# Performance work log

Hardware: AMD Instinct MI355X
Metric: run time of the kernel (lower is better)

## Reference

```python
import jax, jax.numpy as jnp
import numpy as np

NEG_SLOPE = 0.2
EPS = 1e-16


def gatv2_conv(x, src, dst, n_nodes, Wl, Wr, att, bias):
    """GATv2Conv, heads=1, add_self_loops handled by caller via src/dst.
    x: [N, Fin]; src/dst: [E] (message j->i means src=j, dst=i).
    Wl, Wr: [Fin, Fout]; att: [Fout]; bias: [Fout].
    """
    xl = x @ Wl  # [N, Fout] (source transform)
    xr = x @ Wr  # [N, Fout] (target transform)
    # per-edge attention logit: a^T LeakyReLU(xl[j] + xr[i])
    h = xl[src] + xr[dst]                      # [E, Fout]
    e = jax.nn.leaky_relu(h, NEG_SLOPE) @ att  # [E]
    # segment softmax over incoming edges of each dst node
    m = jax.ops.segment_max(e, dst, num_segments=n_nodes)   # [N]
    ex = jnp.exp(e - m[dst])                                 # [E]
    denom = jax.ops.segment_sum(ex, dst, num_segments=n_nodes)  # [N]
    alpha = ex / (denom[dst] + EPS)                          # [E]
    # scatter-aggregate weighted source messages
    out = jax.ops.segment_sum(alpha[:, None] * xl[src], dst, num_segments=n_nodes)
    return out + bias


def glorot(key, shape):
    lim = np.sqrt(6.0 / (shape[0] + shape[1]))
    return jax.random.uniform(key, shape, jnp.float32, -lim, lim)


def setup_inputs() -> dict:
    key = jax.random.key(0)
    ks = jax.random.split(key, 9)
    N, E, Fin, H, Fout = 50000, 800000, 128, 64, 2
    x = jax.random.normal(ks[0], (N, Fin), jnp.float32)
    edge_index = jax.random.randint(ks[1], (2, E), 0, N, jnp.int64)
    return {
        "x": x,
        "edge_index": edge_index,
        "Wl1": glorot(ks[2], (Fin, H)),
        "Wr1": glorot(ks[3], (Fin, H)),
        "att1": glorot(ks[4], (H, 1))[:, 0],
        "b1": jnp.zeros((H,), jnp.float32),
        "Wl2": glorot(ks[5], (H, Fout)),
        "Wr2": glorot(ks[6], (H, Fout)),
        "att2": glorot(ks[7], (Fout, 1))[:, 0],
        "b2": jnp.zeros((Fout,), jnp.float32),
    }


def reference(x, edge_index, Wl1, Wr1, att1, b1, Wl2, Wr2, att2, b2):
    n_nodes = x.shape[0]
    # PyG GATv2Conv adds self-loops by default
    loops = jnp.arange(n_nodes, dtype=edge_index.dtype)
    src = jnp.concatenate([edge_index[0], loops])
    dst = jnp.concatenate([edge_index[1], loops])
    # eval mode: dropout is identity; the initial relu/dropout result is dead code
    h = gatv2_conv(x, src, dst, n_nodes, Wl1, Wr1, att1, b1)
    out = gatv2_conv(h, src, dst, n_nodes, Wl2, Wr2, att2, b2)
    return out
```

## Files before the change

### kernel.cpp

```cpp
#include <hip/hip_runtime.h>
#include <math.h>

#define FIN 128
#define H 64
#define FOUT 2
#define NEG_SLOPE 0.2f
#define EPS 1e-16f

#define BM 64
#define BK 32
#define SCAN_CHUNK 2048

__global__ void k_zero_int(int* __restrict__ a, int n){
  int i = blockIdx.x*blockDim.x + threadIdx.x;
  if(i < n) a[i] = 0;
}

__device__ __forceinline__ void load_bs(const int* __restrict__ blocksum, int nscan,
                                        int* bs, int tid){
  if(tid < 64){
    int v = (tid < nscan)? blocksum[tid] : 0;
    int incl = v;
    #pragma unroll
    for(int o=1;o<64;o<<=1){ int u=__shfl_up(incl,o); if(tid>=o) incl+=u; }
    bs[tid] = incl - v;
  }
  __syncthreads();
}

__global__ __launch_bounds__(256) void k_deg_gemm(
    const int* __restrict__ ei, int E, int Etot,
    int* __restrict__ deg, int* __restrict__ rank, int GD,
    const float* __restrict__ x, const float* __restrict__ Wl,
    const float* __restrict__ Wr, float* __restrict__ xl,
    float* __restrict__ xr, int N){
  __shared__ float xsT[BK][BM+4];
  __shared__ float ws[BK][128];
  int tid = threadIdx.x;

  if((int)blockIdx.x < GD){
    int i0 = (blockIdx.x*256 + tid)*4;
    if(i0 >= Etot) return;
    if(i0 + 4 <= E && (E & 3) == 0){
      int4 d4 = *(const int4*)(ei + E + i0);
      int r0 = atomicAdd(&deg[d4.x],1);
      int r1 = atomicAdd(&deg[d4.y],1);
      int r2 = atomicAdd(&deg[d4.z],1);
      int r3 = atomicAdd(&deg[d4.w],1);
      *(int4*)(rank + i0) = make_int4(r0,r1,r2,r3);
    } else if(i0 >= E && i0 + 4 <= Etot){
      int v = i0 - E;
      int r0 = atomicAdd(&deg[v+0],1);
      int r1 = atomicAdd(&deg[v+1],1);
      int r2 = atomicAdd(&deg[v+2],1);
      int r3 = atomicAdd(&deg[v+3],1);
      *(int4*)(rank + i0) = make_int4(r0,r1,r2,r3);
    } else {
      #pragma unroll
      for(int q=0;q<4;q++){
        int i = i0+q; if(i>=Etot) break;
        int dst = (i<E) ? ei[E+i] : (i-E);
        rank[i] = atomicAdd(&deg[dst],1);
      }
    }
    return;
  }

  int rowbase = (blockIdx.x - GD)*BM;
  int tc = tid & 15, tr = tid >> 4;
  int r0 = tr*4, c0 = tc*4;
  float acc[4][8];
  #pragma unroll
  for(int i=0;i<4;i++)
    #pragma unroll
    for(int j=0;j<8;j++) acc[i][j]=0.f;

  int lrow = tid >> 2;
  int lk8  = (tid & 3) * 8;
  int wkk  = tid >> 3;
  int wfq  = tid & 7;

  for(int k0=0; k0<FIN; k0+=BK){
    __syncthreads();
    {
      int grow = rowbase + lrow;
      float4 v0 = make_float4(0,0,0,0), v1 = make_float4(0,0,0,0);
      if(grow < N){
        v0 = *(const float4*)(x + (size_t)grow*FIN + k0 + lk8);
        v1 = *(const float4*)(x + (size_t)grow*FIN + k0 + lk8 + 4);
      }
      xsT[lk8+0][lrow]=v0.x; xsT[lk8+1][lrow]=v0.y; xsT[lk8+2][lrow]=v0.z; xsT[lk8+3][lrow]=v0.w;
      xsT[lk8+4][lrow]=v1.x; xsT[lk8+5][lrow]=v1.y; xsT[lk8+6][lrow]=v1.z; xsT[lk8+7][lrow]=v1.w;
    }
    #pragma unroll
    for(int i=0;i<4;i++){
      int c4 = (wfq + i*8)*4;
      const float* srcp = (c4 < 64) ? (Wl + (size_t)(k0+wkk)*H + c4)
                                    : (Wr + (size_t)(k0+wkk)*H + (c4-64));
      *(float4*)(&ws[wkk][c4]) = *(const float4*)srcp;
    }
    __syncthreads();
    #pragma unroll
    for(int kk=0; kk<BK; kk++){
      float4 av = *(float4*)(&xsT[kk][r0]);
      float4 b0 = *(float4*)(&ws[kk][c0]);
      float4 b1 = *(float4*)(&ws[kk][64+c0]);
      float a[4] = {av.x,av.y,av.z,av.w};
      float b[8] = {b0.x,b0.y,b0.z,b0.w,b1.x,b1.y,b1.z,b1.w};
      #pragma unroll
      for(int i=0;i<4;i++)
        #pragma unroll
        for(int j=0;j<8;j++)
          acc[i][j] += a[i]*b[j];
    }
  }
  #pragma unroll
  for(int i=0;i<4;i++){
    int row = rowbase + r0 + i;
    if(row < N){
      *(float4*)(xl + (size_t)row*H + c0) = make_float4(acc[i][0],acc[i][1],acc[i][2],acc[i][3]);
      *(float4*)(xr + (size_t)row*H + c0) = make_float4(acc[i][4],acc[i][5],acc[i][6],acc[i][7]);
    }
  }
}

__global__ __launch_bounds__(256) void k_scan_a(const int* __restrict__ deg, int n,
                                                int* __restrict__ rowptr,
                                                int* __restrict__ blocksum){
  __shared__ int wsum[4];
  int tid = threadIdx.x, lane = tid & 63, wid = tid >> 6;
  int idx = blockIdx.x*SCAN_CHUNK + tid*8;
  int v[8];
  if(idx + 8 <= n){
    int4 a = *(const int4*)(deg + idx);
    int4 b = *(const int4*)(deg + idx + 4);
    v[0]=a.x;v[1]=a.y;v[2]=a.z;v[3]=a.w;v[4]=b.x;v[5]=b.y;v[6]=b.z;v[7]=b.w;
  } else {
    #pragma unroll
    for(int i=0;i<8;i++) v[i] = (idx+i<n)? deg[idx+i] : 0;
  }
  int pre[8]; int st=0;
  #pragma unroll
  for(int i=0;i<8;i++){ pre[i]=st; st+=v[i]; }
  int incl = st;
  #pragma unroll
  for(int o=1;o<64;o<<=1){ int u=__shfl_up(incl,o); if(lane>=o) incl+=u; }
  if(lane==63) wsum[wid]=incl;
  __syncthreads();
  if(tid==0){ int accu=0; for(int i=0;i<4;i++){ int t=wsum[i]; wsum[i]=accu; accu+=t; } }
  __syncthreads();
  int toff = wsum[wid] + incl - st;
  if(idx + 8 <= n){
    int4 o0 = make_int4(toff+pre[0],toff+pre[1],toff+pre[2],toff+pre[3]);
    int4 o1 = make_int4(toff+pre[4],toff+pre[5],toff+pre[6],toff+pre[7]);
    *(int4*)(rowptr+idx)=o0; *(int4*)(rowptr+idx+4)=o1;
  } else {
    #pragma unroll
    for(int i=0;i<8;i++) if(idx+i<n) rowptr[idx+i]=toff+pre[i];
  }
  if(tid==255){
    blocksum[blockIdx.x] = toff + st;
    if(blockIdx.x == gridDim.x-1) rowptr[n] = toff + st;
  }
}

__global__ void k_fill(const int* __restrict__ ei, int E, int Etot,
                       const int* __restrict__ rowptr,
                       const int* __restrict__ blocksum, int nscan,
                       const int* __restrict__ rank, int* __restrict__ csr_src){
  __shared__ int bs[64];
  int tid = threadIdx.x;
  load_bs(blocksum, nscan, bs, tid);
  int i0 = (blockIdx.x*blockDim.x + tid)*4;
  if(i0 >= Etot) return;
  if(i0 + 4 <= E && (E & 3) == 0){
    int4 s4 = *(const int4*)(ei + i0);
    int4 d4 = *(const int4*)(ei + E + i0);
    int4 r4 = *(const int4*)(rank + i0);
    csr_src[rowptr[d4.x] + bs[d4.x>>11] + r4.x] = s4.x;
    csr_src[rowptr[d4.y] + bs[d4.y>>11] + r4.y] = s4.y;
    csr_src[rowptr[d4.z] + bs[d4.z>>11] + r4.z] = s4.z;
    csr_src[rowptr[d4.w] + bs[d4.w>>11] + r4.w] = s4.w;
  } else if(i0 >= E && i0 + 4 <= Etot){
    int4 r4 = *(const int4*)(rank + i0);
    int v = i0 - E;
    csr_src[rowptr[v+0] + bs[(v+0)>>11] + r4.x] = v+0;
    csr_src[rowptr[v+1] + bs[(v+1)>>11] + r4.y] = v+1;
    csr_src[rowptr[v+2] + bs[(v+2)>>11] + r4.z] = v+2;
    csr_src[rowptr[v+3] + bs[(v+3)>>11] + r4.w] = v+3;
  } else {
    #pragma unroll
    for(int q=0;q<4;q++){
      int i = i0+q; if(i>=Etot) break;
      int src, dst;
      if(i<E){ src = ei[i]; dst = ei[E+i]; } else { src = i-E; dst = i-E; }
      csr_src[rowptr[dst] + bs[dst>>11] + rank[i]] = src;
    }
  }
}

__global__ void k_node1f(const int* __restrict__ rowptr, const int* __restrict__ blocksum,
                         int nscan, const int* __restrict__ csr_src,
                         const float* __restrict__ xl, const float* __restrict__ xr,
                         const float* __restrict__ att, const float* __restrict__ b1,
                         const float* __restrict__ Wl2, const float* __restrict__ Wr2,
                         float* __restrict__ xl2, float* __restrict__ xr2, int N){
  __shared__ int bs[64];
  int tid = threadIdx.x;
  load_bs(blocksum, nscan, bs, tid);
  int node = blockIdx.x*16 + (tid>>4);
  int gl = tid & 15;
  if(node >= N) return;
  int f4 = gl*4;
  float4 attv = *(const float4*)(att + f4);
  float4 xrv  = *(const float4*)(xr + (size_t)node*H + f4);
  int s = rowptr[node]   + bs[node>>11];
  int t = rowptr[node+1] + bs[(node+1)>>11];
  float d = 0.f;
  float ax=0.f, ay=0.f, az=0.f, aw=0.f;

  for(int k=s; k<t; k+=8){
    int tl = t - 1;
    int ks[8]; float4 xv[8]; float msk[8];
    #pragma unroll
    for(int j=0;j<8;j++){
      int kj = k + j;
      ks[j] = (kj < t) ? kj : tl;
      msk[j] = (kj < t) ? 1.f : 0.f;
    }
    int ss[8];
    #pragma unroll
    for(int j=0;j<8;j++) ss[j] = csr_src[ks[j]];
    #pragma unroll
    for(int j=0;j<8;j++) xv[j] = *(const float4*)(xl + (size_t)ss[j]*H + f4);
    #pragma unroll
    for(int j=0;j<8;j++){
      float h0 = xv[j].x + xrv.x, h1 = xv[j].y + xrv.y;
      float h2 = xv[j].z + xrv.z, h3 = xv[j].w + xrv.w;
      float l0 = (h0>0.f)? h0 : NEG_SLOPE*h0;
      float l1 = (h1>0.f)? h1 : NEG_SLOPE*h1;
      float l2 = (h2>0.f)? h2 : NEG_SLOPE*h2;
      float l3 = (h3>0.f)? h3 : NEG_SLOPE*h3;
      float e = l0*attv.x + l1*attv.y + l2*attv.z + l3*attv.w;
      #pragma unroll
      for(int o=1;o<16;o<<=1) e += __shfl_xor(e,o);
      float w = msk[j] * __expf(e);
      d  += w;
      ax += w*xv[j].x; ay += w*xv[j].y; az += w*xv[j].z; aw += w*xv[j].w;
    }
  }

  float inv = 1.f/(d + EPS);
  float4 bv = *(const float4*)(b1 + f4);
  float h0 = ax*inv + bv.x, h1 = ay*inv + bv.y;
  float h2 = az*inv + bv.z, h3 = aw*inv + bv.w;
  float p0 = h0*Wl2[(f4+0)*FOUT+0] + h1*Wl2[(f4+1)*FOUT+0] + h2*Wl2[(f4+2)*FOUT+0] + h3*Wl2[(f4+3)*FOUT+0];
  float p1 = h0*Wl2[(f4+0)*FOUT+1] + h1*Wl2[(f4+1)*FOUT+1] + h2*Wl2[(f4+2)*FOUT+1] + h3*Wl2[(f4+3)*FOUT+1];
  float p2 = h0*Wr2[(f4+0)*FOUT+0] + h1*Wr2[(f4+1)*FOUT+0] + h2*Wr2[(f4+2)*FOUT+0] + h3*Wr2[(f4+3)*FOUT+0];
  float p3 = h0*Wr2[(f4+0)*FOUT+1] + h1*Wr2[(f4+1)*FOUT+1] + h2*Wr2[(f4+2)*FOUT+1] + h3*Wr2[(f4+3)*FOUT+1];
  #pragma unroll
  for(int o=1;o<16;o<<=1){
    p0 += __shfl_xor(p0,o); p1 += __shfl_xor(p1,o);
    p2 += __shfl_xor(p2,o); p3 += __shfl_xor(p3,o);
  }
  if(gl==0){
    *(float2*)(xl2 + node*2) = make_float2(p0,p1);
    *(float2*)(xr2 + node*2) = make_float2(p2,p3);
  }
}

__global__ void k_node2(const int* __restrict__ rowptr, const int* __restrict__ blocksum,
                        int nscan, const int* __restrict__ csr_src,
                        const float* __restrict__ xl2, const float* __restrict__ xr2,
                        const float* __restrict__ att2, const float* __restrict__ b2,
                        float* __restrict__ out, int N){
  __shared__ int bs[64];
  int tid = threadIdx.x;
  load_bs(blocksum, nscan, bs, tid);
  int node = blockIdx.x*16 + (tid>>4);
  int gl = tid & 15;
  if(node >= N) return;
  int s = rowptr[node]   + bs[node>>11];
  int t = rowptr[node+1] + bs[(node+1)>>11];
  float2 xrv = *(const float2*)(xr2 + node*2);
  float a0 = att2[0], a1 = att2[1];
  float den=0.f, n0=0.f, n1=0.f;
  for(int k=s+gl; k<t; k+=16){
    int src = csr_src[k];
    float2 xs = *(const float2*)(xl2 + src*2);
    float h0 = xs.x + xrv.x, h1 = xs.y + xrv.y;
    float l0 = (h0>0.f)? h0 : NEG_SLOPE*h0;
    float l1 = (h1>0.f)? h1 : NEG_SLOPE*h1;
    float ex = __expf(l0*a0 + l1*a1);
    den += ex; n0 += ex*xs.x; n1 += ex*xs.y;
  }
  #pragma unroll
  for(int o=1;o<16;o<<=1){
    den += __shfl_xor(den,o);
    n0  += __shfl_xor(n0,o);
    n1  += __shfl_xor(n1,o);
  }
  if(gl==0){
    float inv = 1.f/(den + EPS);
    out[node*2+0] = n0*inv + b2[0];
    out[node*2+1] = n1*inv + b2[1];
  }
}

extern "C" void kernel_launch(void* const* d_in, const int* in_sizes, int n_in,
                              void* d_out, int out_size, void* d_ws, size_t ws_size,
                              hipStream_t stream){
  const float* x    = (const float*)d_in[0];
  const int*   ei   = (const int*)d_in[1];
  const float* Wl1  = (const float*)d_in[2];
  const float* Wr1  = (const float*)d_in[3];
  const float* att1 = (const float*)d_in[4];
  const float* b1   = (const float*)d_in[5];
  const float* Wl2  = (const float*)d_in[6];
  const float* Wr2  = (const float*)d_in[7];
  const float* att2 = (const float*)d_in[8];
  const float* b2   = (const float*)d_in[9];
  int N = in_sizes[0]/FIN;
  int E = in_sizes[1]/2;
  int Etot = E + N;
  int nscan = (N + SCAN_CHUNK - 1) / SCAN_CHUNK;
  int nquad = (Etot + 3) / 4;
  int GD = (nquad + 255) / 256;
  int GG = (N + BM - 1) / BM;

  char* w = (char*)d_ws;
  size_t off = 0;
  auto alloc = [&](size_t bytes)->void*{
    void* p = w + off;
    off = (off + bytes + 255) & ~(size_t)255;
    return p;
  };
  float* xl1     = (float*)alloc((size_t)N*H*4);
  float* xr1     = (float*)alloc((size_t)N*H*4);
  int*   csr_src = (int*)  alloc((size_t)Etot*4);
  int*   rank    = (int*)  alloc((size_t)Etot*4);
  int*   deg     = (int*)  alloc((size_t)N*4);
  int*   rowptr  = (int*)  alloc((size_t)(N+1)*4);
  int*   blocksum= (int*)  alloc((size_t)64*4);
  float* xl2     = (float*)alloc((size_t)N*2*4);
  float* xr2     = (float*)alloc((size_t)N*2*4);

  k_zero_int<<<(N+511)/512,512,0,stream>>>(deg, N);
  k_deg_gemm<<<GD+GG, 256, 0, stream>>>(ei, E, Etot, deg, rank, GD,
                                        x, Wl1, Wr1, xl1, xr1, N);
  k_scan_a<<<nscan,256,0,stream>>>(deg, N, rowptr, blocksum);
  k_fill<<<GD,256,0,stream>>>(ei, E, Etot, rowptr, blocksum, nscan, rank, csr_src);
  k_node1f<<<(N+15)/16, 256, 0, stream>>>(rowptr, blocksum, nscan, csr_src,
                                          xl1, xr1, att1, b1, Wl2, Wr2, xl2, xr2, N);
  k_node2<<<(N+15)/16, 256, 0, stream>>>(rowptr, blocksum, nscan, csr_src,
                                         xl2, xr2, att2, b2, (float*)d_out, N);
}
```

Baseline: 130.5 us.

## Replace FP32 SIMT GEMM with split-bf16 MFMA GEMM and separate degree kernel

The first-layer projection x@[Wl|Wr] moves from an FP32 shared-memory SIMT GEMM to MFMA bf16 instructions. Both operands are split into high and residual bf16 parts and three products are summed, which keeps accuracy close to FP32. A prep kernel pre-packs the weights into the MFMA operand layout and also zeros the degree array, replacing the separate zero kernel. The degree-counting atomics, previously fused into the GEMM launch, now run as their own kernel after the GEMM, so the two no longer overlap and there is one more launch.

Measured after the change: 128.8 us. About the same (-1.3%).

```diff
diff --git a/kernel.cpp b/kernel.cpp
--- a/kernel.cpp
+++ b/kernel.cpp
@@ -7,14 +7,10 @@
 #define NEG_SLOPE 0.2f
 #define EPS 1e-16f
 
-#define BM 64
-#define BK 32
 #define SCAN_CHUNK 2048
 
-__global__ void k_zero_int(int* __restrict__ a, int n){
-  int i = blockIdx.x*blockDim.x + threadIdx.x;
-  if(i < n) a[i] = 0;
-}
+typedef __attribute__((ext_vector_type(8))) short s8v;
+typedef __attribute__((ext_vector_type(4))) float f4v;
 
 __device__ __forceinline__ void load_bs(const int* __restrict__ blocksum, int nscan,
                                         int* bs, int tid){
@@ -28,98 +24,111 @@
   __syncthreads();
 }
 
-__global__ __launch_bounds__(256) void k_deg_gemm(
-    const int* __restrict__ ei, int E, int Etot,
-    int* __restrict__ deg, int* __restrict__ rank, int GD,
-    const float* __restrict__ x, const float* __restrict__ Wl,
-    const float* __restrict__ Wr, float* __restrict__ xl,
-    float* __restrict__ xr, int N){
-  __shared__ float xsT[BK][BM+4];
-  __shared__ float ws[BK][128];
+__global__ void k_prep(int* __restrict__ deg, int N, int ZB,
+                       const float* __restrict__ Wl, const float* __restrict__ Wr,
+                       unsigned short* __restrict__ pWh, unsigned short* __restrict__ pWe){
+  int b = blockIdx.x;
+  if(b < ZB){
+    int i = b*256 + threadIdx.x;
+    if(i < N) deg[i] = 0;
+    return;
+  }
+  int idx = (b - ZB)*256 + threadIdx.x;
+  int lane = idx & 63;
+  int ctk  = idx >> 6;
+  int k0   = (ctk & 3) * 32;
+  int ct   = ctk >> 2;
+  int c    = ct*16 + (lane & 15);
+  int kb   = k0 + (lane >> 4)*8;
+  const float* Wp = (c < 64) ? (Wl + c) : (Wr + (c - 64));
+  #pragma unroll
+  for(int j=0;j<8;j++){
+    float v = Wp[(size_t)(kb + j)*H];
+    unsigned u = __float_as_uint(v);
+    unsigned short hb = (unsigned short)(u >> 16);
+    float hv = __uint_as_float(((unsigned)hb) << 16);
+    float ev = v - hv;
+    unsigned short eb = (unsigned short)(__float_as_uint(ev) >> 16);
+    pWh[(size_t)idx*8 + j] = hb;
+    pWe[(size_t)idx*8 + j] = eb;
+  }
+}
+
+__global__ __launch_bounds__(256) void k_gemm_mfma(
+    const float* __restrict__ x,
+    const unsigned short* __restrict__ pWh, const unsigned short* __restrict__ pWe,
+    float* __restrict__ xl, float* __restrict__ xr, int N){
   int tid = threadIdx.x;
-
-  if((int)blockIdx.x < GD){
-    int i0 = (blockIdx.x*256 + tid)*4;
-    if(i0 >= Etot) return;
-    if(i0 + 4 <= E && (E & 3) == 0){
-      int4 d4 = *(const int4*)(ei + E + i0);
-      int r0 = atomicAdd(&deg[d4.x],1);
-      int r1 = atomicAdd(&deg[d4.y],1);
-      int r2 = atomicAdd(&deg[d4.z],1);
-      int r3 = atomicAdd(&deg[d4.w],1);
-      *(int4*)(rank + i0) = make_int4(r0,r1,r2,r3);
-    } else if(i0 >= E && i0 + 4 <= Etot){
-      int v = i0 - E;
-      int r0 = atomicAdd(&deg[v+0],1);
-      int r1 = atomicAdd(&deg[v+1],1);
-      int r2 = atomicAdd(&deg[v+2],1);
-      int r3 = atomicAdd(&deg[v+3],1);
-      *(int4*)(rank + i0) = make_int4(r0,r1,r2,r3);
-    } else {
-      #pragma unroll
-      for(int q=0;q<4;q++){
-        int i = i0+q; if(i>=Etot) break;
-        int dst = (i<E) ? ei[E+i] : (i-E);
-        rank[i] = atomicAdd(&deg[dst],1);
-      }
-    }
-    return;
-  }
-
-  int rowbase = (blockIdx.x - GD)*BM;
-  int tc = tid & 15, tr = tid >> 4;
-  int r0 = tr*4, c0 = tc*4;
-  float acc[4][8];
-  #pragma unroll
-  for(int i=0;i<4;i++)
-    #pragma unroll
-    for(int j=0;j<8;j++) acc[i][j]=0.f;
-
-  int lrow = tid >> 2;
-  int lk8  = (tid & 3) * 8;
-  int wkk  = tid >> 3;
-  int wfq  = tid & 7;
-
-  for(int k0=0; k0<FIN; k0+=BK){
-    __syncthreads();
-    {
-      int grow = rowbase + lrow;
-      float4 v0 = make_float4(0,0,0,0), v1 = make_float4(0,0,0,0);
-      if(grow < N){
-        v0 = *(const float4*)(x + (size_t)grow*FIN + k0 + lk8);
-        v1 = *(const float4*)(x + (size_t)grow*FIN + k0 + lk8 + 4);
-      }
-      xsT[lk8+0][lrow]=v0.x; xsT[lk8+1][lrow]=v0.y; xsT[lk8+2][lrow]=v0.z; xsT[lk8+3][lrow]=v0.w;
-      xsT[lk8+4][lrow]=v1.x; xsT[lk8+5][lrow]=v1.y; xsT[lk8+6][lrow]=v1.z; xsT[lk8+7][lrow]=v1.w;
-    }
-    #pragma unroll
-    for(int i=0;i<4;i++){
-      int c4 = (wfq + i*8)*4;
-      const float* srcp = (c4 < 64) ? (Wl + (size_t)(k0+wkk)*H + c4)
-                                    : (Wr + (size_t)(k0+wkk)*H + (c4-64));
-      *(float4*)(&ws[wkk][c4]) = *(const float4*)srcp;
-    }
-    __syncthreads();
-    #pragma unroll
-    for(int kk=0; kk<BK; kk++){
-      float4 av = *(float4*)(&xsT[kk][r0]);
-      float4 b0 = *(float4*)(&ws[kk][c0]);
-      float4 b1 = *(float4*)(&ws[kk][64+c0]);
-      float a[4] = {av.x,av.y,av.z,av.w};
-      float b[8] = {b0.x,b0.y,b0.z,b0.w,b1.x,b1.y,b1.z,b1.w};
-      #pragma unroll
-      for(int i=0;i<4;i++)
-        #pragma unroll
-        for(int j=0;j<8;j++)
-          acc[i][j] += a[i]*b[j];
-    }
-  }
-  #pragma unroll
-  for(int i=0;i<4;i++){
-    int row = rowbase + r0 + i;
-    if(row < N){
-      *(float4*)(xl + (size_t)row*H + c0) = make_float4(acc[i][0],acc[i][1],acc[i][2],acc[i][3]);
-      *(float4*)(xr + (size_t)row*H + c0) = make_float4(acc[i][4],acc[i][5],acc[i][6],acc[i][7]);
+  int lane = tid & 63, wid = tid >> 6;
+  int rowbase = blockIdx.x*64 + wid*16;
+  int r = lane & 15, g = lane >> 4;
+  f4v acc[8];
+  #pragma unroll
+  for(int ct=0;ct<8;ct++) acc[ct] = (f4v){0.f,0.f,0.f,0.f};
+
+  int arow = rowbase + r; if(arow > N-1) arow = N-1;
+  const float* xrow = x + (size_t)arow*FIN;
+
+  #pragma unroll
+  for(int k0=0;k0<4;k0++){
+    float4 va = *(const float4*)(xrow + k0*32 + g*8);
+    float4 vb = *(const float4*)(xrow + k0*32 + g*8 + 4);
+    float xs_[8] = {va.x,va.y,va.z,va.w,vb.x,vb.y,vb.z,vb.w};
+    s8v ah, ae;
+    #pragma unroll
+    for(int j=0;j<8;j++){
+      unsigned u = __float_as_uint(xs_[j]);
+      unsigned short hb = (unsigned short)(u >> 16);
+      ah[j] = (short)hb;
+      float ev = xs_[j] - __uint_as_float(((unsigned)hb) << 16);
+      ae[j] = (short)(unsigned short)(__float_as_uint(ev) >> 16);
+    }
+    #pragma unroll
+    for(int ct=0;ct<8;ct++){
+      size_t boff = ((size_t)(ct*4 + k0)*64 + lane)*8;
+      s8v bh = *(const s8v*)(pWh + boff);
+      s8v be = *(const s8v*)(pWe + boff);
+      acc[ct] = __builtin_amdgcn_mfma_f32_16x16x32_bf16(ah, bh, acc[ct], 0,0,0);
+      acc[ct] = __builtin_amdgcn_mfma_f32_16x16x32_bf16(ah, be, acc[ct], 0,0,0);
+      acc[ct] = __builtin_amdgcn_mfma_f32_16x16x32_bf16(ae, bh, acc[ct], 0,0,0);
+    }
+  }
+  #pragma unroll
+  for(int ct=0;ct<8;ct++){
+    float* dst = (ct < 4) ? xl : xr;
+    int cc = (ct & 3)*16 + r;
+    #pragma unroll
+    for(int rr=0;rr<4;rr++){
+      int row = rowbase + g*4 + rr;
+      if(row < N) dst[(size_t)row*H + cc] = acc[ct][rr];
+    }
+  }
+}
+
+__global__ void k_degree(const int* __restrict__ ei, int E, int Etot,
+                         int* __restrict__ deg, int* __restrict__ rank){
+  int i0 = (blockIdx.x*blockDim.x + threadIdx.x)*4;
+  if(i0 >= Etot) return;
+  if(i0 + 4 <= E && (E & 3) == 0){
+    int4 d4 = *(const int4*)(ei + E + i0);
+    int r0 = atomicAdd(&deg[d4.x],1);
+    int r1 = atomicAdd(&deg[d4.y],1);
+    int r2 = atomicAdd(&deg[d4.z],1);
+    int r3 = atomicAdd(&deg[d4.w],1);
+    *(int4*)(rank + i0) = make_int4(r0,r1,r2,r3);
+  } else if(i0 >= E && i0 + 4 <= Etot){
+    int v = i0 - E;
+    int r0 = atomicAdd(&deg[v+0],1);
+    int r1 = atomicAdd(&deg[v+1],1);
+    int r2 = atomicAdd(&deg[v+2],1);
+    int r3 = atomicAdd(&deg[v+3],1);
+    *(int4*)(rank + i0) = make_int4(r0,r1,r2,r3);
+  } else {
+    #pragma unroll
+    for(int q=0;q<4;q++){
+      int i = i0+q; if(i>=Etot) break;
+      int dst = (i<E) ? ei[E+i] : (i-E);
+      rank[i] = atomicAdd(&deg[dst],1);
     }
   }
 }
@@ -325,8 +334,7 @@
   int Etot = E + N;
   int nscan = (N + SCAN_CHUNK - 1) / SCAN_CHUNK;
   int nquad = (Etot + 3) / 4;
-  int GD = (nquad + 255) / 256;
-  int GG = (N + BM - 1) / BM;
+  int ZB = (N + 255) / 256;
 
   char* w = (char*)d_ws;
   size_t off = 0;
@@ -344,12 +352,14 @@
   int*   blocksum= (int*)  alloc((size_t)64*4);
   float* xl2     = (float*)alloc((size_t)N*2*4);
   float* xr2     = (float*)alloc((size_t)N*2*4);
-
-  k_zero_int<<<(N+511)/512,512,0,stream>>>(deg, N);
-  k_deg_gemm<<<GD+GG, 256, 0, stream>>>(ei, E, Etot, deg, rank, GD,
-                                        x, Wl1, Wr1, xl1, xr1, N);
+  unsigned short* pWh = (unsigned short*)alloc((size_t)2048*8*2);
+  unsigned short* pWe = (unsigned short*)alloc((size_t)2048*8*2);
+
+  k_prep<<<ZB+8, 256, 0, stream>>>(deg, N, ZB, Wl1, Wr1, pWh, pWe);
+  k_gemm_mfma<<<(N+63)/64, 256, 0, stream>>>(x, pWh, pWe, xl1, xr1, N);
+  k_degree<<<(nquad+255)/256,256,0,stream>>>(ei, E, Etot, deg, rank);
   k_scan_a<<<nscan,256,0,stream>>>(deg, N, rowptr, blocksum);
-  k_fill<<<GD,256,0,stream>>>(ei, E, Etot, rowptr, blocksum, nscan, rank, csr_src);
+  k_fill<<<(nquad+255)/256,256,0,stream>>>(ei, E, Etot, rowptr, blocksum, nscan, rank, csr_src);
   k_node1f<<<(N+15)/16, 256, 0, stream>>>(rowptr, blocksum, nscan, csr_src,
                                           xl1, xr1, att1, b1, Wl2, Wr2, xl2, xr2, N);
   k_node2<<<(N+15)/16, 256, 0, stream>>>(rowptr, blocksum, nscan, csr_src,
```
